# Optimization experiments

Measured on AMD Instinct MI355X. Metric: run time of the kernel, lower is better.

Reference implementation:

```python
import jax, jax.numpy as jnp
import numpy as np

B, N, C, H = 4, 2048, 1024, 16
HD = C // H  # head_dim = 64


def setup_inputs() -> dict:
    key = jax.random.key(0)
    ks = jax.random.split(key, 16)
    s = 0.02
    return {
        "x": jax.random.normal(ks[0], (B, N, C), dtype=jnp.float32),
        # qkv_proj: Linear(C, 3C): weight (3C, C), bias (3C,)
        "W_qkv": jax.random.normal(ks[1], (3 * C, C), dtype=jnp.float32) * s,
        "b_qkv": jax.random.normal(ks[2], (3 * C,), dtype=jnp.float32) * s,
        # out_proj: Linear(C, C)
        "W_out": jax.random.normal(ks[3], (C, C), dtype=jnp.float32) * s,
        "b_out": jax.random.normal(ks[4], (C,), dtype=jnp.float32) * s,
        # dynamically-reassigned position bias: shape (1, N, H, H) per the code's
        # (B, num_heads=N, seq_len=H, seq_len=H) score tensor
        "pos_bias": jax.random.normal(ks[5], (1, N, H, H), dtype=jnp.float32) * 0.01,
        # conv_proj: Linear(C, C)
        "W_cp": jax.random.normal(ks[6], (C, C), dtype=jnp.float32) * s,
        "b_cp": jax.random.normal(ks[7], (C,), dtype=jnp.float32) * s,
        # pointwise Conv1d(C, C, k=1): weight (C, C) after squeezing kernel dim
        "W_pw": jax.random.normal(ks[8], (C, C), dtype=jnp.float32) * s,
        "b_pw": jax.random.normal(ks[9], (C,), dtype=jnp.float32) * s,
        # depthwise Conv1d(C, C, k=3, groups=C): weight (C, 3)
        "W_dw": jax.random.normal(ks[10], (C, 3), dtype=jnp.float32) * s,
        "b_dw": jax.random.normal(ks[11], (C,), dtype=jnp.float32) * s,
        # token_wise_proj: Linear(C, C)
        "W_tw": jax.random.normal(ks[12], (C, C), dtype=jnp.float32) * s,
        "b_tw": jax.random.normal(ks[13], (C,), dtype=jnp.float32) * s,
    }


def reference(x, W_qkv, b_qkv, W_out, b_out, pos_bias, W_cp, b_cp,
              W_pw, b_pw, W_dw, b_dw, W_tw, b_tw) -> jnp.ndarray:
    Bx, Nx, Cx = x.shape
    scale = HD ** -0.5
    # qkv -> (B, N, H, 3*HD), chunk into q,k,v of (B, N, H, HD).
    # NOTE: faithful to the torch code, heads stay on axis 2; the matmul
    # contracts head_dim giving (B, N, H, H) scores (attention over heads).
    qkv = (x @ W_qkv.T + b_qkv).reshape(Bx, Nx, H, 3 * HD)
    q, k, v = jnp.split(qkv, 3, axis=-1)
    scores = jnp.einsum('bnhd,bngd->bnhg', q, k) * scale + pos_bias
    attn = jax.nn.softmax(scores, axis=-1)
    attn_out = jnp.einsum('bnhg,bngd->bnhd', attn, v).reshape(Bx, Nx, Cx)
    attn_out = attn_out @ W_out.T + b_out

    # Convolutional branch
    xc = x @ W_cp.T + b_cp          # conv_proj
    xc = xc @ W_pw.T + b_pw          # pointwise conv (k=1) == linear over channels
    xp = jnp.pad(xc, ((0, 0), (1, 1), (0, 0)))  # pad seq for k=3, padding=1
    xc = (xp[:, :-2] * W_dw[:, 0] + xp[:, 1:-1] * W_dw[:, 1]
          + xp[:, 2:] * W_dw[:, 2] + b_dw)      # depthwise conv
    xc = xc @ W_tw.T + b_tw          # token_wise_proj

    return attn_out + xc
```

## Files before the change

### kernel.cpp

```cpp
#include <hip/hip_runtime.h>
#include <hip/hip_bf16.h>
#include <stdint.h>

typedef __bf16 bf16_t;
typedef __attribute__((ext_vector_type(8))) __bf16 bf16x8;
typedef __attribute__((ext_vector_type(4))) __bf16 bf16x4;
typedef __attribute__((ext_vector_type(4))) float floatx4;

#define GLDS16(g, l)                                                          \
  __builtin_amdgcn_global_load_lds(                                           \
      (const __attribute__((address_space(1))) void*)(g),                     \
      (__attribute__((address_space(3))) void*)(l), 16, 0, 0)

template <typename OT>
__global__ __launch_bounds__(256) void gemm_bt(
    const bf16_t* __restrict__ A, const bf16_t* __restrict__ B,
    const float* __restrict__ bias, OT* __restrict__ C, int M, int N, int K) {
  __shared__ bf16_t As[128 * 64];
  __shared__ bf16_t Bs[128 * 64];
  const int tid = threadIdx.x;
  const int wave = tid >> 6;
  const int lane = tid & 63;
  const int quad = lane >> 4;
  const int l16 = lane & 15;
  const int m0 = blockIdx.x * 128;
  const int n0 = blockIdx.y * 128;
  const int wm = (wave >> 1) * 64;
  const int wn = (wave & 1) * 64;

  const int r0 = wave * 32 + (lane >> 3);
  const int g = ((lane & 7) ^ (r0 & 7)) * 8;
  const bf16_t* Ab = A + (size_t)(m0 + r0) * K + g;
  const bf16_t* Bb = B + (size_t)(n0 + r0) * K + g;

  const int p0 = ((quad ^ (l16 & 7))) * 8;

  floatx4 acc[4][4];
  const floatx4 zf = {0.f, 0.f, 0.f, 0.f};
#pragma unroll
  for (int i = 0; i < 4; ++i)
#pragma unroll
    for (int j = 0; j < 4; ++j) acc[i][j] = zf;

  for (int k0 = 0; k0 < K; k0 += 64) {
#pragma unroll
    for (int t = 0; t < 4; ++t) {
      GLDS16(Ab + (size_t)(t * 8) * K + k0, As + (wave * 256 + t * 64) * 8);
      GLDS16(Bb + (size_t)(t * 8) * K + k0, Bs + (wave * 256 + t * 64) * 8);
    }
    __syncthreads();
#pragma unroll
    for (int ks = 0; ks < 2; ++ks) {
      const int ko = p0 ^ (ks * 32);
      bf16x8 af[4], bfr[4];
#pragma unroll
      for (int i = 0; i < 4; ++i)
        af[i] = *(const bf16x8*)(As + (wm + i * 16 + l16) * 64 + ko);
#pragma unroll
      for (int j = 0; j < 4; ++j)
        bfr[j] = *(const bf16x8*)(Bs + (wn + j * 16 + l16) * 64 + ko);
#pragma unroll
      for (int i = 0; i < 4; ++i)
#pragma unroll
        for (int j = 0; j < 4; ++j)
          acc[i][j] = __builtin_amdgcn_mfma_f32_16x16x32_bf16(
              bfr[j], af[i], acc[i][j], 0, 0, 0);
    }
    __syncthreads();
  }

#pragma unroll
  for (int j = 0; j < 4; ++j) {
    const int colb = n0 + wn + j * 16 + quad * 4;
    floatx4 bv = zf;
    if (bias) bv = *(const floatx4*)(bias + colb);
#pragma unroll
    for (int i = 0; i < 4; ++i) {
      const int row = m0 + wm + i * 16 + l16;
      floatx4 v = acc[i][j] + bv;
      if constexpr (sizeof(OT) == 4) {
        *(floatx4*)((float*)C + (size_t)row * N + colb) = v;
      } else {
        union {
          bf16_t b[4];
          uint32_t u[2];
        } pk;
        pk.b[0] = (bf16_t)v[0];
        pk.b[1] = (bf16_t)v[1];
        pk.b[2] = (bf16_t)v[2];
        pk.b[3] = (bf16_t)v[3];
        uint32_t* dst = (uint32_t*)((bf16_t*)C + (size_t)row * N + colb);
        dst[0] = pk.u[0];
        dst[1] = pk.u[1];
      }
    }
  }
}

__global__ __launch_bounds__(256) void prep_k(
    const float* __restrict__ x, bf16_t* __restrict__ x_bf,
    const float* __restrict__ Wqkv, bf16_t* __restrict__ Wbig1,
    const float* __restrict__ Wpw, bf16_t* __restrict__ Wpw_bf,
    const float* __restrict__ Wout, const float* __restrict__ Wtw,
    bf16_t* __restrict__ Wbig2, const float* __restrict__ bqkv,
    float* __restrict__ bias1, const float* __restrict__ bout,
    const float* __restrict__ btw, float* __restrict__ bias2) {
  const int b = blockIdx.x, tid = threadIdx.x;
  auto cvt4 = [](const float* in, bf16_t* out, int i) {
    floatx4 v = ((const floatx4*)in)[i];
    bf16x4 o;
    o[0] = (bf16_t)v[0];
    o[1] = (bf16_t)v[1];
    o[2] = (bf16_t)v[2];
    o[3] = (bf16_t)v[3];
    ((bf16x4*)out)[i] = o;
  };
  if (b < 8192) {
    cvt4(x, x_bf, b * 256 + tid);
  } else if (b < 11264) {
    cvt4(Wqkv, Wbig1, (b - 8192) * 256 + tid);
  } else if (b < 12288) {
    cvt4(Wpw, Wpw_bf, (b - 11264) * 256 + tid);
  } else if (b < 14336) {
    const bool second = b >= 13312;
    int i = (b - (second ? 13312 : 12288)) * 256 + tid;
    floatx4 v = ((const floatx4*)(second ? Wtw : Wout))[i];
    bf16x4 o;
    o[0] = (bf16_t)v[0];
    o[1] = (bf16_t)v[1];
    o[2] = (bf16_t)v[2];
    o[3] = (bf16_t)v[3];
    int row = i >> 8, c4 = i & 255;
    *(bf16x4*)(Wbig2 + (size_t)row * 2048 + (second ? 1024 : 0) + c4 * 4) = o;
  } else if (b < 14339) {
    int i = (b - 14336) * 256 + tid;
    if (i < 768) ((floatx4*)bias1)[i] = ((const floatx4*)bqkv)[i];
  } else {
    ((floatx4*)bias2)[tid] =
        ((const floatx4*)bout)[tid] + ((const floatx4*)btw)[tid];
  }
}

__global__ __launch_bounds__(256) void transpose_cvt_k(
    const float* __restrict__ in, bf16_t* __restrict__ out) {
  __shared__ float t[32][33];
  const int bx = blockIdx.x * 32, by = blockIdx.y * 32;
  const int tx = threadIdx.x, ty = threadIdx.y;
#pragma unroll
  for (int i = 0; i < 32; i += 8)
    t[ty + i][tx] = in[(size_t)(by + ty + i) * 1024 + bx + tx];
  __syncthreads();
#pragma unroll
  for (int i = 0; i < 32; i += 8)
    out[(size_t)(bx + ty + i) * 1024 + by + tx] = (bf16_t)t[tx][ty + i];
}

__global__ __launch_bounds__(64) void bcomb_k(const float* __restrict__ Wpw,
                                              const float* __restrict__ bcp,
                                              const float* __restrict__ bpw,
                                              float* __restrict__ outb) {
  const int i = blockIdx.x;
  const int l = threadIdx.x;
  const float* row = Wpw + (size_t)i * 1024;
  float s = 0.f;
  for (int j = l; j < 1024; j += 64) s += row[j] * bcp[j];
#pragma unroll
  for (int o = 32; o > 0; o >>= 1) s += __shfl_down(s, o);
  if (l == 0) outb[i] = s + bpw[i];
}

static __device__ inline void exp8(uint32_t w0, uint32_t w1, uint32_t w2,
                                   uint32_t w3, float* f) {
  f[0] = __uint_as_float(w0 << 16);
  f[1] = __uint_as_float(w0 & 0xffff0000u);
  f[2] = __uint_as_float(w1 << 16);
  f[3] = __uint_as_float(w1 & 0xffff0000u);
  f[4] = __uint_as_float(w2 << 16);
  f[5] = __uint_as_float(w2 & 0xffff0000u);
  f[6] = __uint_as_float(w3 << 16);
  f[7] = __uint_as_float(w3 & 0xffff0000u);
}

__global__ __launch_bounds__(256) void attn_k(const bf16_t* __restrict__ qkv,
                                              const float* __restrict__ pos,
                                              bf16_t* __restrict__ outp,
                                              int qstride, int ostride) {
  __shared__ float sh[4 * 3264 + 4 * 272];
  const int tid = threadIdx.x;
  const int wave = tid >> 6, lane = tid & 63;
  const int p = blockIdx.x * 4 + wave;
  float* shw = sh + wave * 3264;
  float* pl = sh + 4 * 3264 + wave * 272;

  const uint4* src = (const uint4*)(qkv + (size_t)p * qstride);
#pragma unroll
  for (int i = 0; i < 6; ++i) {
    uint4 w = src[lane + i * 64];
    int c0 = 8 * (lane + i * 64);
    int h = c0 / 192;
    int rem = c0 - h * 192;
    int role = rem >> 6, d0 = rem & 63;
    float f[8];
    exp8(w.x, w.y, w.z, w.w, f);
    float* dst = shw + (h * 3 + role) * 68 + d0;
    *(floatx4*)dst = *(floatx4*)f;
    *(floatx4*)(dst + 4) = *(floatx4*)(f + 4);
  }
  __syncthreads();

  const int l16 = lane & 15, quad = lane >> 4;
  const int h = l16, g0 = quad * 4;
  const float* qrow = shw + h * 204;
  const float* krow = shw + (g0 * 3 + 1) * 68;
  const floatx4 zf = {0.f, 0.f, 0.f, 0.f};
  floatx4 s4[4] = {zf, zf, zf, zf};
  for (int d = 0; d < 64; d += 4) {
    floatx4 qv = *(const floatx4*)(qrow + d);
    s4[0] += qv * *(const floatx4*)(krow + d);
    s4[1] += qv * *(const floatx4*)(krow + 204 + d);
    s4[2] += qv * *(const floatx4*)(krow + 408 + d);
    s4[3] += qv * *(const floatx4*)(krow + 612 + d);
  }
  const float* pb = pos + (size_t)(p & 2047) * 256 + h * 16 + g0;
  float s[4];
#pragma unroll
  for (int jj = 0; jj < 4; ++jj)
    s[jj] = (s4[jj][0] + s4[jj][1] + s4[jj][2] + s4[jj][3]) * 0.125f + pb[jj];

  float m = fmaxf(fmaxf(s[0], s[1]), fmaxf(s[2], s[3]));
  m = fmaxf(m, __shfl_xor(m, 16));
  m = fmaxf(m, __shfl_xor(m, 32));
  float e[4], sum = 0.f;
#pragma unroll
  for (int jj = 0; jj < 4; ++jj) {
    e[jj] = __expf(s[jj] - m);
    sum += e[jj];
  }
  sum += __shfl_xor(sum, 16);
  sum += __shfl_xor(sum, 32);
  const float inv = 1.0f / sum;
#pragma unroll
  for (int jj = 0; jj < 4; ++jj) pl[h * 17 + g0 + jj] = e[jj] * inv;
  __syncthreads();

  const int h2 = lane >> 2, dbase = (lane & 3) * 16;
  floatx4 o0 = zf, o1 = zf, o2 = zf, o3 = zf;
  for (int g = 0; g < 16; ++g) {
    float pw = pl[h2 * 17 + g];
    const float* vr = shw + g * 204 + 136 + dbase;
    o0 += pw * *(const floatx4*)(vr);
    o1 += pw * *(const floatx4*)(vr + 4);
    o2 += pw * *(const floatx4*)(vr + 8);
    o3 += pw * *(const floatx4*)(vr + 12);
  }
  union {
    bf16_t b[16];
    uint4 u4[2];
  } pk;
#pragma unroll
  for (int t2 = 0; t2 < 4; ++t2) {
    pk.b[t2] = (bf16_t)o0[t2];
    pk.b[4 + t2] = (bf16_t)o1[t2];
    pk.b[8 + t2] = (bf16_t)o2[t2];
    pk.b[12 + t2] = (bf16_t)o3[t2];
  }
  uint4* dst = (uint4*)(outp + (size_t)p * ostride + h2 * 64 + dbase);
  dst[0] = pk.u4[0];
  dst[1] = pk.u4[1];
}

__global__ __launch_bounds__(256) void dwconv_k(const bf16_t* __restrict__ in,
                                                const float* __restrict__ Wdw,
                                                const float* __restrict__ bdw,
                                                bf16_t* __restrict__ out) {
  const int item = blockIdx.x * 256 + threadIdx.x;
  const int cc = item & 127, rowg = item >> 7;
  const int c0 = cc * 8;
  float w0[8], w1[8], w2[8], bb[8];
#pragma unroll
  for (int c = 0; c < 8; ++c) {
    w0[c] = Wdw[(c0 + c) * 3];
    w1[c] = Wdw[(c0 + c) * 3 + 1];
    w2[c] = Wdw[(c0 + c) * 3 + 2];
    bb[c] = bdw[c0 + c];
  }
#pragma unroll
  for (int jr = 0; jr < 4; ++jr) {
    const int t = rowg * 4 + jr;
    const int n = t & 2047;
    const bf16_t* ip = in + (size_t)t * 4096 + c0;
    const uint4 z4 = {0, 0, 0, 0};
    uint4 um = (n > 0) ? *(const uint4*)(ip - 4096) : z4;
    uint4 uc = *(const uint4*)(ip);
    uint4 up = (n < 2047) ? *(const uint4*)(ip + 4096) : z4;
    float fm[8], fc[8], fp[8];
    exp8(um.x, um.y, um.z, um.w, fm);
    exp8(uc.x, uc.y, uc.z, uc.w, fc);
    exp8(up.x, up.y, up.z, up.w, fp);
    union {
      bf16_t b[8];
      uint4 u;
    } pk;
#pragma unroll
    for (int c = 0; c < 8; ++c)
      pk.b[c] = (bf16_t)(bb[c] + fm[c] * w0[c] + fc[c] * w1[c] + fp[c] * w2[c]);
    *(uint4*)(out + (size_t)t * 2048 + c0) = pk.u;
  }
}

extern "C" void kernel_launch(void* const* d_in, const int* in_sizes, int n_in,
                              void* d_out, int out_size, void* d_ws,
                              size_t ws_size, hipStream_t stream) {
  (void)in_sizes; (void)n_in; (void)out_size; (void)ws_size;
  const float* x = (const float*)d_in[0];
  const float* Wqkv = (const float*)d_in[1];
  const float* bqkv = (const float*)d_in[2];
  const float* Wout = (const float*)d_in[3];
  const float* bout = (const float*)d_in[4];
  const float* pos = (const float*)d_in[5];
  const float* Wcp = (const float*)d_in[6];
  const float* bcp = (const float*)d_in[7];
  const float* Wpw = (const float*)d_in[8];
  const float* bpw = (const float*)d_in[9];
  const float* Wdw = (const float*)d_in[10];
  const float* bdw = (const float*)d_in[11];
  const float* Wtw = (const float*)d_in[12];
  const float* btw = (const float*)d_in[13];
  float* out = (float*)d_out;

  char* ws = (char*)d_ws;
  const size_t MB = 1024ull * 1024ull;
  bf16_t* x_bf = (bf16_t*)(ws + 0);
  bf16_t* Wbig1 = (bf16_t*)(ws + 16 * MB);
  bf16_t* WcpT = (bf16_t*)(ws + 24 * MB);
  bf16_t* Wpw_bf = (bf16_t*)(ws + 26 * MB);
  bf16_t* Mid = (bf16_t*)(ws + 0);
  bf16_t* Wbig2 = (bf16_t*)(ws + 32 * MB);
  float* bias1 = (float*)(ws + 36 * MB);
  float* bias2 = (float*)(ws + 36 * MB + 65536);
  bf16_t* G1out = (bf16_t*)(ws + 37 * MB);

  prep_k<<<14340, 256, 0, stream>>>(x, x_bf, Wqkv, Wbig1, Wpw, Wpw_bf, Wout,
                                    Wtw, Wbig2, bqkv, bias1, bout, btw, bias2);
  transpose_cvt_k<<<dim3(32, 32), dim3(32, 8), 0, stream>>>(Wcp, WcpT);
  bcomb_k<<<1024, 64, 0, stream>>>(Wpw, bcp, bpw, bias1 + 3072);

  gemm_bt<bf16_t><<<dim3(8, 8), 256, 0, stream>>>(
      Wpw_bf, WcpT, nullptr, Wbig1 + (size_t)3072 * 1024, 1024, 1024, 1024);

  gemm_bt<bf16_t><<<dim3(64, 32), 256, 0, stream>>>(
      x_bf, Wbig1, bias1, G1out, 8192, 4096, 1024);

  attn_k<<<2048, 256, 0, stream>>>(G1out, pos, Mid, 4096, 2048);
  dwconv_k<<<1024, 256, 0, stream>>>(G1out + 3072, Wdw, bdw, Mid + 1024);

  gemm_bt<float><<<dim3(64, 8), 256, 0, stream>>>(Mid, Wbig2, bias2, out,
                                                  8192, 1024, 2048);
}
```

Measured before the change: 309.6 us.

## Use MFMA for head-attention and stage bf16 GEMM epilogue through LDS

The per-token attention over heads is rewritten to compute the 16x16 scores and the P·V product with MFMA instructions, reading q/k/v straight from global memory instead of unpacking them into LDS as fp32. Separately, the bf16-output GEMM epilogue now writes its tile into swizzled shared memory and then stores full 16-byte rows coalesced to global. Both target memory inefficiency: LDS staging and scalar FMA work in attention, and scattered 8-byte stores in the GEMM output. The risks are fp16 rounding of the probabilities and V values, strided scalar V loads, and one extra barrier in the GEMM epilogue.

```diff
diff --git a/kernel.cpp b/kernel.cpp
--- a/kernel.cpp
+++ b/kernel.cpp
@@ -6,6 +6,7 @@
 typedef __attribute__((ext_vector_type(8))) __bf16 bf16x8;
 typedef __attribute__((ext_vector_type(4))) __bf16 bf16x4;
 typedef __attribute__((ext_vector_type(4))) float floatx4;
+typedef __attribute__((ext_vector_type(4))) _Float16 half4_t;
 
 #define GLDS16(g, l)                                                          \
   __builtin_amdgcn_global_load_lds(                                           \
@@ -16,8 +17,9 @@
 __global__ __launch_bounds__(256) void gemm_bt(
     const bf16_t* __restrict__ A, const bf16_t* __restrict__ B,
     const float* __restrict__ bias, OT* __restrict__ C, int M, int N, int K) {
-  __shared__ bf16_t As[128 * 64];
-  __shared__ bf16_t Bs[128 * 64];
+  __shared__ bf16_t sm[128 * 128];
+  bf16_t* As = sm;
+  bf16_t* Bs = sm + 128 * 64;
   const int tid = threadIdx.x;
   const int wave = tid >> 6;
   const int lane = tid & 63;
@@ -32,7 +34,6 @@
   const int g = ((lane & 7) ^ (r0 & 7)) * 8;
   const bf16_t* Ab = A + (size_t)(m0 + r0) * K + g;
   const bf16_t* Bb = B + (size_t)(n0 + r0) * K + g;
-
   const int p0 = ((quad ^ (l16 & 7))) * 8;
 
   floatx4 acc[4][4];
@@ -69,30 +70,52 @@
     __syncthreads();
   }
 
-#pragma unroll
-  for (int j = 0; j < 4; ++j) {
-    const int colb = n0 + wn + j * 16 + quad * 4;
-    floatx4 bv = zf;
-    if (bias) bv = *(const floatx4*)(bias + colb);
-#pragma unroll
-    for (int i = 0; i < 4; ++i) {
-      const int row = m0 + wm + i * 16 + l16;
-      floatx4 v = acc[i][j] + bv;
-      if constexpr (sizeof(OT) == 4) {
+  if constexpr (sizeof(OT) == 4) {
+#pragma unroll
+    for (int j = 0; j < 4; ++j) {
+      const int colb = n0 + wn + j * 16 + quad * 4;
+      floatx4 bv = zf;
+      if (bias) bv = *(const floatx4*)(bias + colb);
+#pragma unroll
+      for (int i = 0; i < 4; ++i) {
+        const int row = m0 + wm + i * 16 + l16;
+        floatx4 v = acc[i][j] + bv;
         *(floatx4*)((float*)C + (size_t)row * N + colb) = v;
-      } else {
+      }
+    }
+  } else {
+#pragma unroll
+    for (int j = 0; j < 4; ++j) {
+      const int colb = n0 + wn + j * 16 + quad * 4;
+      floatx4 bv = zf;
+      if (bias) bv = *(const floatx4*)(bias + colb);
+      const int gcol = ((wn + j * 16 + quad * 4) >> 2);
+#pragma unroll
+      for (int i = 0; i < 4; ++i) {
+        const int rl = wm + i * 16 + l16;
+        floatx4 v = acc[i][j] + bv;
         union {
           bf16_t b[4];
-          uint32_t u[2];
+          uint2 u2;
         } pk;
         pk.b[0] = (bf16_t)v[0];
         pk.b[1] = (bf16_t)v[1];
         pk.b[2] = (bf16_t)v[2];
         pk.b[3] = (bf16_t)v[3];
-        uint32_t* dst = (uint32_t*)((bf16_t*)C + (size_t)row * N + colb);
-        dst[0] = pk.u[0];
-        dst[1] = pk.u[1];
+        const int gsw = gcol ^ ((rl & 7) * 4);
+        *(uint2*)(sm + rl * 128 + gsw * 4) = pk.u2;
       }
+    }
+    __syncthreads();
+    bf16_t* Cb = (bf16_t*)C;
+#pragma unroll
+    for (int pass = 0; pass < 8; ++pass) {
+      const int f = pass * 256 + tid;
+      const int row = f >> 4;
+      const int c16 = f & 15;
+      const int g0 = (2 * c16) ^ ((row & 7) * 4);
+      uint4 v = *(const uint4*)(sm + row * 128 + g0 * 4);
+      *(uint4*)(Cb + (size_t)(m0 + row) * N + n0 + c16 * 8) = v;
     }
   }
 }
@@ -169,6 +192,65 @@
   if (l == 0) outb[i] = s + bpw[i];
 }
 
+__global__ __launch_bounds__(256) void attn_k(const bf16_t* __restrict__ qkv,
+                                              const float* __restrict__ pos,
+                                              bf16_t* __restrict__ outp) {
+  const int tid = threadIdx.x;
+  const int wave = tid >> 6, lane = tid & 63;
+  const int p = blockIdx.x * 4 + wave;
+  const int l16 = lane & 15, quad = lane >> 4;
+  const bf16_t* row = qkv + (size_t)p * 4096;
+  const bf16_t* qb = row + l16 * 192 + quad * 8;
+
+  bf16x8 q0 = *(const bf16x8*)(qb);
+  bf16x8 q1 = *(const bf16x8*)(qb + 32);
+  bf16x8 k0 = *(const bf16x8*)(qb + 64);
+  bf16x8 k1 = *(const bf16x8*)(qb + 96);
+  floatx4 S = {0.f, 0.f, 0.f, 0.f};
+  S = __builtin_amdgcn_mfma_f32_16x16x32_bf16(k0, q0, S, 0, 0, 0);
+  S = __builtin_amdgcn_mfma_f32_16x16x32_bf16(k1, q1, S, 0, 0, 0);
+
+  const floatx4 pb =
+      *(const floatx4*)(pos + (size_t)(p & 2047) * 256 + l16 * 16 + quad * 4);
+  float v[4];
+#pragma unroll
+  for (int r = 0; r < 4; ++r) v[r] = S[r] * 0.125f + pb[r];
+
+  float m = fmaxf(fmaxf(v[0], v[1]), fmaxf(v[2], v[3]));
+  m = fmaxf(m, __shfl_xor(m, 16));
+  m = fmaxf(m, __shfl_xor(m, 32));
+  float e[4], sum = 0.f;
+#pragma unroll
+  for (int r = 0; r < 4; ++r) {
+    e[r] = __expf(v[r] - m);
+    sum += e[r];
+  }
+  sum += __shfl_xor(sum, 16);
+  sum += __shfl_xor(sum, 32);
+  const float inv = 1.0f / sum;
+  half4_t pa;
+#pragma unroll
+  for (int r = 0; r < 4; ++r) pa[r] = (_Float16)(e[r] * inv);
+
+  const bf16_t* vb_base = row + 128 + l16;
+  const floatx4 zf = {0.f, 0.f, 0.f, 0.f};
+  floatx4 o[4];
+#pragma unroll
+  for (int t = 0; t < 4; ++t) {
+    half4_t vb;
+#pragma unroll
+    for (int j = 0; j < 4; ++j)
+      vb[j] = (_Float16)(float)vb_base[(quad * 4 + j) * 192 + t * 16];
+    o[t] = __builtin_amdgcn_mfma_f32_16x16x16f16(pa, vb, zf, 0, 0, 0);
+  }
+
+  bf16_t* ob = outp + (size_t)p * 2048 + (quad * 4) * 64 + l16;
+#pragma unroll
+  for (int r = 0; r < 4; ++r)
+#pragma unroll
+    for (int t = 0; t < 4; ++t) ob[r * 64 + t * 16] = (bf16_t)o[t][r];
+}
+
 static __device__ inline void exp8(uint32_t w0, uint32_t w1, uint32_t w2,
                                    uint32_t w3, float* f) {
   f[0] = __uint_as_float(w0 << 16);
@@ -179,94 +261,6 @@
   f[5] = __uint_as_float(w2 & 0xffff0000u);
   f[6] = __uint_as_float(w3 << 16);
   f[7] = __uint_as_float(w3 & 0xffff0000u);
-}
-
-__global__ __launch_bounds__(256) void attn_k(const bf16_t* __restrict__ qkv,
-                                              const float* __restrict__ pos,
-                                              bf16_t* __restrict__ outp,
-                                              int qstride, int ostride) {
-  __shared__ float sh[4 * 3264 + 4 * 272];
-  const int tid = threadIdx.x;
-  const int wave = tid >> 6, lane = tid & 63;
-  const int p = blockIdx.x * 4 + wave;
-  float* shw = sh + wave * 3264;
-  float* pl = sh + 4 * 3264 + wave * 272;
-
-  const uint4* src = (const uint4*)(qkv + (size_t)p * qstride);
-#pragma unroll
-  for (int i = 0; i < 6; ++i) {
-    uint4 w = src[lane + i * 64];
-    int c0 = 8 * (lane + i * 64);
-    int h = c0 / 192;
-    int rem = c0 - h * 192;
-    int role = rem >> 6, d0 = rem & 63;
-    float f[8];
-    exp8(w.x, w.y, w.z, w.w, f);
-    float* dst = shw + (h * 3 + role) * 68 + d0;
-    *(floatx4*)dst = *(floatx4*)f;
-    *(floatx4*)(dst + 4) = *(floatx4*)(f + 4);
-  }
-  __syncthreads();
-
-  const int l16 = lane & 15, quad = lane >> 4;
-  const int h = l16, g0 = quad * 4;
-  const float* qrow = shw + h * 204;
-  const float* krow = shw + (g0 * 3 + 1) * 68;
-  const floatx4 zf = {0.f, 0.f, 0.f, 0.f};
-  floatx4 s4[4] = {zf, zf, zf, zf};
-  for (int d = 0; d < 64; d += 4) {
-    floatx4 qv = *(const floatx4*)(qrow + d);
-    s4[0] += qv * *(const floatx4*)(krow + d);
-    s4[1] += qv * *(const floatx4*)(krow + 204 + d);
-    s4[2] += qv * *(const floatx4*)(krow + 408 + d);
-    s4[3] += qv * *(const floatx4*)(krow + 612 + d);
-  }
-  const float* pb = pos + (size_t)(p & 2047) * 256 + h * 16 + g0;
-  float s[4];
-#pragma unroll
-  for (int jj = 0; jj < 4; ++jj)
-    s[jj] = (s4[jj][0] + s4[jj][1] + s4[jj][2] + s4[jj][3]) * 0.125f + pb[jj];
-
-  float m = fmaxf(fmaxf(s[0], s[1]), fmaxf(s[2], s[3]));
-  m = fmaxf(m, __shfl_xor(m, 16));
-  m = fmaxf(m, __shfl_xor(m, 32));
-  float e[4], sum = 0.f;
-#pragma unroll
-  for (int jj = 0; jj < 4; ++jj) {
-    e[jj] = __expf(s[jj] - m);
-    sum += e[jj];
-  }
-  sum += __shfl_xor(sum, 16);
-  sum += __shfl_xor(sum, 32);
-  const float inv = 1.0f / sum;
-#pragma unroll
-  for (int jj = 0; jj < 4; ++jj) pl[h * 17 + g0 + jj] = e[jj] * inv;
-  __syncthreads();
-
-  const int h2 = lane >> 2, dbase = (lane & 3) * 16;
-  floatx4 o0 = zf, o1 = zf, o2 = zf, o3 = zf;
-  for (int g = 0; g < 16; ++g) {
-    float pw = pl[h2 * 17 + g];
-    const float* vr = shw + g * 204 + 136 + dbase;
-    o0 += pw * *(const floatx4*)(vr);
-    o1 += pw * *(const floatx4*)(vr + 4);
-    o2 += pw * *(const floatx4*)(vr + 8);
-    o3 += pw * *(const floatx4*)(vr + 12);
-  }
-  union {
-    bf16_t b[16];
-    uint4 u4[2];
-  } pk;
-#pragma unroll
-  for (int t2 = 0; t2 < 4; ++t2) {
-    pk.b[t2] = (bf16_t)o0[t2];
-    pk.b[4 + t2] = (bf16_t)o1[t2];
-    pk.b[8 + t2] = (bf16_t)o2[t2];
-    pk.b[12 + t2] = (bf16_t)o3[t2];
-  }
-  uint4* dst = (uint4*)(outp + (size_t)p * ostride + h2 * 64 + dbase);
-  dst[0] = pk.u4[0];
-  dst[1] = pk.u4[1];
 }
 
 __global__ __launch_bounds__(256) void dwconv_k(const bf16_t* __restrict__ in,
@@ -351,7 +345,7 @@
   gemm_bt<bf16_t><<<dim3(64, 32), 256, 0, stream>>>(
       x_bf, Wbig1, bias1, G1out, 8192, 4096, 1024);
 
-  attn_k<<<2048, 256, 0, stream>>>(G1out, pos, Mid, 4096, 2048);
+  attn_k<<<2048, 256, 0, stream>>>(G1out, pos, Mid);
   dwconv_k<<<1024, 256, 0, stream>>>(G1out + 3072, Wdw, bdw, Mid + 1024);
 
   gemm_bt<float><<<dim3(64, 8), 256, 0, stream>>>(Mid, Wbig2, bias2, out,
```

Result: faster. 295.6 us (-4.5%).
